# Optimization experiments

Hardware: AMD Instinct MI355X
Metric: run time of the kernel (lower is better)

## Reference

```python
import jax, jax.numpy as jnp
import numpy as np

B, M, H, E, N_ITEMS, N_USERS = 1024, 50, 128, 128, 100000, 1000


def setup_inputs() -> dict:
    key = jax.random.key(0)
    ks = jax.random.split(key, 16)
    s = 0.05
    return {
        "input_embedding": jax.random.normal(ks[0], (B, 1, E), jnp.float32),
        "hidden": jax.random.normal(ks[1], (1, B, H), jnp.float32),
        "inter_output": jax.random.normal(ks[2], (B, M, H), jnp.float32),
        "delta_t_h": jax.random.uniform(ks[3], (B,), jnp.float32),
        "user_list": jax.random.randint(ks[4], (B,), 0, N_USERS),
        # GRU params (input size 2*E since use_attn, single layer)
        "gru_w_ih": jax.random.normal(ks[5], (3 * H, 2 * E), jnp.float32) * s,
        "gru_w_hh": jax.random.normal(ks[6], (3 * H, H), jnp.float32) * s,
        "gru_b_ih": jax.random.normal(ks[7], (3 * H,), jnp.float32) * s,
        "gru_b_hh": jax.random.normal(ks[8], (3 * H,), jnp.float32) * s,
        # output projection
        "lin_W": jax.random.normal(ks[9], (N_ITEMS, H), jnp.float32) * s,
        "lin_b": jax.random.normal(ks[10], (N_ITEMS,), jnp.float32) * s,
        # per-user expert params ('cat' attention path)
        "cat_W": jax.random.normal(ks[11], (N_USERS, H, 2 * H), jnp.float32) * s,
        "cat_b": jax.random.normal(ks[12], (N_USERS, H), jnp.float32) * s,
        "scale_W": jax.random.normal(ks[13], (N_USERS, 1, H), jnp.float32) * s,
        "scale_b": jax.random.normal(ks[14], (N_USERS, 1), jnp.float32) * s,
    }


def reference(input_embedding, hidden, inter_output, delta_t_h, user_list,
              gru_w_ih, gru_w_hh, gru_b_ih, gru_b_hh,
              lin_W, lin_b, cat_W, cat_b, scale_W, scale_b):
    b, m, h = inter_output.shape
    # dropout in eval mode (p effectively 0) -> identity
    embedded_input = input_embedding
    hidden_t = jnp.transpose(hidden, (1, 0, 2))            # [B,1,H]
    # per-user 'cat' attention: gather each example's expert weights
    cat_in = jnp.concatenate(
        [jnp.broadcast_to(hidden_t, (b, m, h)), inter_output], axis=2)  # [B,M,2H]
    Wc = cat_W[user_list]                                   # [B,H,2H]
    bc = cat_b[user_list]                                   # [B,H]
    result = jnp.tanh(jnp.einsum('bmi,bhi->bmh', cat_in, Wc) + bc[:, None, :])
    Ws = scale_W[user_list]                                 # [B,1,H]
    bs = scale_b[user_list]                                 # [B,1]
    energies = jnp.einsum('bmh,boh->bmo', result, Ws) + bs[:, None, :]  # [B,M,1]
    attn_weights = jax.nn.softmax(energies[..., 0], axis=1)             # [B,M]
    context = jnp.einsum('bm,bmh->bh', attn_weights, inter_output)[:, None, :]  # [B,1,H]
    gru_in = jnp.concatenate([embedded_input, context], axis=2)         # [B,1,2E]
    # single-step GRU (PyTorch gate layout: r, z, n)
    x = gru_in[:, 0, :]
    h0 = hidden[0]                                          # [B,H]
    gi = x @ gru_w_ih.T + gru_b_ih                          # [B,3H]
    gh = h0 @ gru_w_hh.T + gru_b_hh
    i_r, i_z, i_n = jnp.split(gi, 3, axis=1)
    h_r, h_z, h_n = jnp.split(gh, 3, axis=1)
    r = jax.nn.sigmoid(i_r + h_r)
    z = jax.nn.sigmoid(i_z + h_z)
    n = jnp.tanh(i_n + r * h_n)
    h_new = (1.0 - z) * n + z * h0                          # [B,H]
    gru_output = h_new[:, None, :]                          # [B,1,H]
    output = gru_output @ lin_W.T + lin_b                   # [B,1,N_ITEMS]
    return (output, h_new[None], embedded_input, gru_output, attn_weights)
```

## Files before the change

kernel.cpp:

```cpp
#include <hip/hip_runtime.h>
#include <math.h>

#define NB 1024
#define NM 50
#define NH 128
#define NI 100000

constexpr size_t OFF_H   = (size_t)NB * NI;
constexpr size_t OFF_EMB = OFF_H   + (size_t)NB * NH;
constexpr size_t OFF_GRU = OFF_EMB + (size_t)NB * NH;
constexpr size_t OFF_ATT = OFF_GRU + (size_t)NB * NH;

#define CONV_BLOCKS 512

typedef __attribute__((ext_vector_type(8))) short bf16x8;
typedef __attribute__((ext_vector_type(4))) float f32x4;

static __device__ __forceinline__ unsigned short f2bf(float x) {
    unsigned int u = __float_as_uint(x);
    return (unsigned short)((u + 0x7FFFu + ((u >> 16) & 1u)) >> 16);
}
static __device__ __forceinline__ float bf2f(unsigned short v) {
    return __uint_as_float((unsigned int)v << 16);
}
static __device__ __forceinline__ float fast_tanh(float x) {
    float cx = fminf(fmaxf(x, -15.0f), 15.0f);
    float e = __expf(2.0f * cx);
    return (e - 1.0f) / (e + 1.0f);
}
static __device__ __forceinline__ float fast_sigmoid(float x) {
    float cx = fminf(fmaxf(x, -30.0f), 30.0f);
    return 1.0f / (1.0f + __expf(-cx));
}
static __device__ __forceinline__ bf16x8 pack8(float4 f0, float4 f1) {
    bf16x8 p;
    p[0] = (short)f2bf(f0.x); p[1] = (short)f2bf(f0.y);
    p[2] = (short)f2bf(f0.z); p[3] = (short)f2bf(f0.w);
    p[4] = (short)f2bf(f1.x); p[5] = (short)f2bf(f1.y);
    p[6] = (short)f2bf(f1.z); p[7] = (short)f2bf(f1.w);
    return p;
}

template<bool PRE>
__global__ __launch_bounds__(256) void attn_conv_split(
    const float* __restrict__ hidden,
    const float* __restrict__ inter,
    const int*   __restrict__ user_list,
    const float* __restrict__ cat_W,
    const float* __restrict__ cat_b,
    const float* __restrict__ scale_W,
    const float* __restrict__ lin_W,
    unsigned short* __restrict__ Wbf,
    float* __restrict__ attn_out,
    float* __restrict__ context)
{
    const int tid = threadIdx.x;

    if (blockIdx.x < CONV_BLOCKS) {
        if (PRE) {
            const int n8 = NI * NH / 8;
            for (int i = blockIdx.x * 256 + tid; i < n8; i += CONV_BLOCKS * 256) {
                const float* s = lin_W + (size_t)i * 8;
                bf16x8 p = pack8(*(const float4*)s, *(const float4*)(s + 4));
                __builtin_nontemporal_store(p, reinterpret_cast<bf16x8*>(Wbf + (size_t)i * 8));
            }
        }
        return;
    }

    const int b    = blockIdx.x - CONV_BLOCKS;
    const int lane = tid & 63;
    const int wave = tid >> 6;

    __shared__ __align__(16) unsigned short A[64 * 256];
    __shared__ float e_sm[64];
    __shared__ float attn_sm[64];

    const int u = user_list[b];

    for (int c = tid; c < 2048; c += 256) {
        int r = c >> 5, s = c & 31;
        float4 f0, f1;
        if (s < 16) {
            const float* src = hidden + (size_t)b * NH + s * 8;
            f0 = *(const float4*)src; f1 = *(const float4*)(src + 4);
        } else if (r < NM) {
            const float* src = inter + ((size_t)b * NM + r) * NH + (s - 16) * 8;
            f0 = *(const float4*)src; f1 = *(const float4*)(src + 4);
        } else {
            f0 = (float4){0,0,0,0}; f1 = f0;
        }
        int byte = (r * 512 + s * 16) ^ ((r & 7) << 4);
        *reinterpret_cast<bf16x8*>((char*)A + byte) = pack8(f0, f1);
    }
    if (tid < 64) e_sm[tid] = 0.0f;
    __syncthreads();

    const int lrow = lane & 15;
    const int lk8  = (lane >> 4) * 8;

    float bc[2], ws[2];
    #pragma unroll
    for (int nf = 0; nf < 2; ++nf) {
        int h = wave * 32 + nf * 16 + lrow;
        bc[nf] = cat_b[(size_t)u * NH + h];
        ws[nf] = scale_W[(size_t)u * NH + h];
    }

    f32x4 acc[4][2];
    #pragma unroll
    for (int mf = 0; mf < 4; ++mf)
        #pragma unroll
        for (int nf = 0; nf < 2; ++nf)
            acc[mf][nf] = (f32x4){0,0,0,0};

    #pragma unroll
    for (int ks = 0; ks < 8; ++ks) {
        bf16x8 bfr[2];
        #pragma unroll
        for (int nf = 0; nf < 2; ++nf) {
            int h = wave * 32 + nf * 16 + lrow;
            const float* wp = cat_W + ((size_t)u * NH + h) * 256 + ks * 32 + lk8;
            bfr[nf] = pack8(*(const float4*)wp, *(const float4*)(wp + 4));
        }
        #pragma unroll
        for (int mf = 0; mf < 4; ++mf) {
            int row  = mf * 16 + lrow;
            int byte = (row * 512 + ks * 64 + lk8 * 2) ^ ((row & 7) << 4);
            bf16x8 a = *reinterpret_cast<const bf16x8*>((char*)A + byte);
            acc[mf][0] = __builtin_amdgcn_mfma_f32_16x16x32_bf16(a, bfr[0], acc[mf][0], 0, 0, 0);
            acc[mf][1] = __builtin_amdgcn_mfma_f32_16x16x32_bf16(a, bfr[1], acc[mf][1], 0, 0, 0);
        }
    }

    #pragma unroll
    for (int mf = 0; mf < 4; ++mf) {
        #pragma unroll
        for (int j = 0; j < 4; ++j) {
            float s = fast_tanh(acc[mf][0][j] + bc[0]) * ws[0]
                    + fast_tanh(acc[mf][1][j] + bc[1]) * ws[1];
            s += __shfl_xor(s, 1); s += __shfl_xor(s, 2);
            s += __shfl_xor(s, 4); s += __shfl_xor(s, 8);
            if (lrow == 0) atomicAdd(&e_sm[mf * 16 + (lane >> 4) * 4 + j], s);
        }
    }
    __syncthreads();

    if (tid < 64) {
        float x = (tid < NM) ? e_sm[tid] : -INFINITY;
        float mx = x;
        #pragma unroll
        for (int s = 1; s < 64; s <<= 1) mx = fmaxf(mx, __shfl_xor(mx, s));
        float ex = (tid < NM) ? __expf(x - mx) : 0.0f;
        float sum = ex;
        #pragma unroll
        for (int s = 1; s < 64; s <<= 1) sum += __shfl_xor(sum, s);
        float aw = ex / sum;
        attn_sm[tid] = aw;
        if (tid < NM) attn_out[(size_t)b * NM + tid] = aw;
    }
    __syncthreads();

    if (tid < NH) {
        float c = 0.0f;
        #pragma unroll
        for (int m = 0; m < NM; ++m) {
            int byte = (m * 512 + (NH + tid) * 2) ^ ((m & 7) << 4);
            c = fmaf(attn_sm[m], bf2f(*reinterpret_cast<const unsigned short*>((char*)A + byte)), c);
        }
        context[(size_t)b * NH + tid] = c;
    }
}

__global__ __launch_bounds__(128) void gru_mfma(
    const float* __restrict__ emb,
    const float* __restrict__ hidden,
    const float* __restrict__ context,
    const float* __restrict__ w_ih,
    const float* __restrict__ w_hh,
    const float* __restrict__ b_ih,
    const float* __restrict__ b_hh,
    float* __restrict__ out_h,
    float* __restrict__ out_emb,
    float* __restrict__ out_gru)
{
    const int bg   = blockIdx.x >> 2;
    const int hc   = blockIdx.x & 3;
    const int b0   = bg * 16;
    const int h0   = hc * 32;
    const int tid  = threadIdx.x;
    const int lane = tid & 63;
    const int wave = tid >> 6;

    __shared__ __align__(16) unsigned short Xs[16 * 256];
    __shared__ __align__(16) unsigned short Hs[16 * 128];
    __shared__ float Gi[96][17];
    __shared__ float Gh[96][17];

    for (int c = tid; c < 768; c += 128) {
        if (c < 512) {
            int r = c >> 5, s = c & 31;
            const float* src = (s < 16)
                ? emb     + (size_t)(b0 + r) * NH + s * 8
                : context + (size_t)(b0 + r) * NH + (s - 16) * 8;
            int byte = (r * 512 + s * 16) ^ ((r & 7) << 4);
            *reinterpret_cast<bf16x8*>((char*)Xs + byte) =
                pack8(*(const float4*)src, *(const float4*)(src + 4));
        } else {
            int cc = c - 512;
            int r = cc >> 4, s = cc & 15;
            const float* src = hidden + (size_t)(b0 + r) * NH + s * 8;
            int byte = (r * 256 + s * 16) ^ ((r & 7) << 4);
            *reinterpret_cast<bf16x8*>((char*)Hs + byte) =
                pack8(*(const float4*)src, *(const float4*)(src + 4));
        }
    }
    __syncthreads();

    const int lrow = lane & 15;
    const int g16  = lane >> 4;
    const int lk8  = g16 * 8;

    bf16x8 xa[8], ha[4];
    #pragma unroll
    for (int ks = 0; ks < 8; ++ks) {
        int byte = (lrow * 512 + ks * 64 + lk8 * 2) ^ ((lrow & 7) << 4);
        xa[ks] = *reinterpret_cast<const bf16x8*>((char*)Xs + byte);
    }
    #pragma unroll
    for (int ks = 0; ks < 4; ++ks) {
        int byte = (lrow * 256 + ks * 64 + lk8 * 2) ^ ((lrow & 7) << 4);
        ha[ks] = *reinterpret_cast<const bf16x8*>((char*)Hs + byte);
    }

    #pragma unroll
    for (int f = 0; f < 3; ++f) {
        const int lb = (wave * 3 + f) * 16;
        const int l  = lb + lrow;
        const int gt = l >> 5;
        const int n  = gt * NH + h0 + (l & 31);
        f32x4 ai = (f32x4){0,0,0,0};
        f32x4 ah = (f32x4){0,0,0,0};
        const float* wi = w_ih + (size_t)n * 256;
        #pragma unroll
        for (int ks = 0; ks < 8; ++ks) {
            const float* wp = wi + ks * 32 + lk8;
            bf16x8 bv = pack8(*(const float4*)wp, *(const float4*)(wp + 4));
            ai = __builtin_amdgcn_mfma_f32_16x16x32_bf16(bv, xa[ks], ai, 0, 0, 0);
        }
        const float* wh = w_hh + (size_t)n * NH;
        #pragma unroll
        for (int ks = 0; ks < 4; ++ks) {
            const float* wp = wh + ks * 32 + lk8;
            bf16x8 bv = pack8(*(const float4*)wp, *(const float4*)(wp + 4));
            ah = __builtin_amdgcn_mfma_f32_16x16x32_bf16(bv, ha[ks], ah, 0, 0, 0);
        }
        #pragma unroll
        for (int j = 0; j < 4; ++j) {
            int lr = lb + g16 * 4 + j;
            Gi[lr][lrow] = ai[j];
            Gh[lr][lrow] = ah[j];
        }
    }
    __syncthreads();

    #pragma unroll
    for (int k = 0; k < 4; ++k) {
        int idx = k * 128 + tid;
        int bb  = idx >> 5;
        int hh  = idx & 31;
        int h   = h0 + hh;
        float gr = Gi[hh][bb]      + b_ih[h];
        float gz = Gi[32 + hh][bb] + b_ih[NH + h];
        float gn = Gi[64 + hh][bb] + b_ih[2 * NH + h];
        float hr = Gh[hh][bb]      + b_hh[h];
        float hz = Gh[32 + hh][bb] + b_hh[NH + h];
        float hn = Gh[64 + hh][bb] + b_hh[2 * NH + h];
        float r = fast_sigmoid(gr + hr);
        float z = fast_sigmoid(gz + hz);
        float n = fast_tanh(gn + r * hn);
        size_t o = (size_t)(b0 + bb) * NH + h;
        float h0v = hidden[o];
        float hnew = (1.0f - z) * n + z * h0v;
        out_h[o]   = hnew;
        out_gru[o] = hnew;
        out_emb[o] = emb[o];
    }
}

template<bool PRE>
__global__ __launch_bounds__(256, 4) void out_mfma(
    const float* __restrict__ hnew,
    const float* __restrict__ lin_W,
    const unsigned short* __restrict__ Wbf,
    const float* __restrict__ lin_b,
    float* __restrict__ out)
{
    const int L  = blockIdx.x;
    const int wg = (L & 7) * 782 + (L >> 3);
    const int mb = wg & 15;
    const int nb = wg >> 4;

    const int tid  = threadIdx.x;
    const int lane = tid & 63;
    const int wave = tid >> 6;

    const int b0 = mb * 64;
    const int n0 = nb * 256 + wave * 64;

    __shared__ __align__(16) unsigned char smem[32 * 260 * 4];
    unsigned short* As = (unsigned short*)smem;
    float (*Cs)[260]   = (float(*)[260])smem;

    for (int c = tid; c < 1024; c += 256) {
        int r = c >> 4;
        int s = c & 15;
        const float* src = hnew + (size_t)(b0 + r) * NH + s * 8;
        bf16x8 p = pack8(*(const float4*)src, *(const float4*)(src + 4));
        int byte = (r * 256 + s * 16) ^ ((r & 7) << 4);
        *reinterpret_cast<bf16x8*>((char*)As + byte) = p;
    }
    __syncthreads();

    const int lrow = lane & 15;
    const int g    = lane >> 4;
    const int lk8  = g * 8;

    f32x4 acc[4][4];
    #pragma unroll
    for (int mf = 0; mf < 4; ++mf)
        #pragma unroll
        for (int nf = 0; nf < 4; ++nf)
            acc[mf][nf] = (f32x4){0,0,0,0};

    #pragma unroll
    for (int ks = 0; ks < 4; ++ks) {
        bf16x8 av[4];
        #pragma unroll
        for (int mf = 0; mf < 4; ++mf) {
            int row  = mf * 16 + lrow;
            int byte = (row * 256 + ks * 64 + lk8 * 2) ^ ((row & 7) << 4);
            av[mf] = *reinterpret_cast<const bf16x8*>((char*)As + byte);
        }
        bf16x8 bv[4];
        #pragma unroll
        for (int nf = 0; nf < 4; ++nf) {
            int n = n0 + nf * 16 + lrow;
            const size_t nrow = (size_t)(n < NI ? n : 0) * NH;
            if (PRE) {
                bv[nf] = *reinterpret_cast<const bf16x8*>(Wbf + nrow + ks * 32 + lk8);
            } else {
                const float* wr = lin_W + nrow + ks * 32 + lk8;
                bv[nf] = pack8(*(const float4*)wr, *(const float4*)(wr + 4));
            }
        }
        #pragma unroll
        for (int nf = 0; nf < 4; ++nf)
            #pragma unroll
            for (int mf = 0; mf < 4; ++mf)
                acc[mf][nf] = __builtin_amdgcn_mfma_f32_16x16x32_bf16(
                    bv[nf], av[mf], acc[mf][nf], 0, 0, 0);
    }

    f32x4 bias4[4];
    #pragma unroll
    for (int nf = 0; nf < 4; ++nf) {
        int nq = n0 + nf * 16 + g * 4;
        if (nq > NI - 4) nq = NI - 4;
        const float4 bv = *(const float4*)(&lin_b[nq]);
        bias4[nf] = (f32x4){bv.x, bv.y, bv.z, bv.w};
    }

    #pragma unroll
    for (int half = 0; half < 2; ++half) {
        __syncthreads();
        #pragma unroll
        for (int mf2 = 0; mf2 < 2; ++mf2) {
            int mf = half * 2 + mf2;
            int rloc = mf2 * 16 + lrow;
            #pragma unroll
            for (int nf = 0; nf < 4; ++nf) {
                int colq = wave * 64 + nf * 16 + g * 4;
                *(f32x4*)(&Cs[rloc][colq]) = acc[mf][nf] + bias4[nf];
            }
        }
        __syncthreads();
        #pragma unroll
        for (int p = 0; p < 8; ++p) {
            int rloc = p * 4 + wave;
            int col4 = lane * 4;
            int n    = nb * 256 + col4;
            if (n < NI) {
                f32x4 v = *(const f32x4*)(&Cs[rloc][col4]);
                __builtin_nontemporal_store(v,
                    (f32x4*)(&out[(size_t)(b0 + half * 32 + rloc) * NI + n]));
            }
        }
    }
}

extern "C" void kernel_launch(void* const* d_in, const int* in_sizes, int n_in,
                              void* d_out, int out_size, void* d_ws, size_t ws_size,
                              hipStream_t stream) {
    const float* emb      = (const float*)d_in[0];
    const float* hidden   = (const float*)d_in[1];
    const float* inter    = (const float*)d_in[2];
    const int*   user     = (const int*)  d_in[4];
    const float* w_ih     = (const float*)d_in[5];
    const float* w_hh     = (const float*)d_in[6];
    const float* b_ih     = (const float*)d_in[7];
    const float* b_hh     = (const float*)d_in[8];
    const float* lin_W    = (const float*)d_in[9];
    const float* lin_b    = (const float*)d_in[10];
    const float* cat_W    = (const float*)d_in[11];
    const float* cat_b    = (const float*)d_in[12];
    const float* scale_W  = (const float*)d_in[13];

    float* out = (float*)d_out;
    const size_t wbf_bytes = (size_t)NI * NH * 2;
    const size_t need = wbf_bytes + 512 * 1024;
    const bool pre = (ws_size >= need);

    unsigned short* Wbf = (unsigned short*)d_ws;
    float* ctx = pre ? (float*)((char*)d_ws + wbf_bytes) : (float*)d_ws;

    if (pre) {
        attn_conv_split<true><<<CONV_BLOCKS + NB, 256, 0, stream>>>(
            hidden, inter, user, cat_W, cat_b, scale_W, lin_W, Wbf,
            out + OFF_ATT, ctx);
        gru_mfma<<<256, 128, 0, stream>>>(emb, hidden, ctx, w_ih, w_hh, b_ih, b_hh,
                                          out + OFF_H, out + OFF_EMB, out + OFF_GRU);
        out_mfma<true><<<6256, 256, 0, stream>>>(out + OFF_H, lin_W, Wbf, lin_b, out);
    } else {
        attn_conv_split<false><<<CONV_BLOCKS + NB, 256, 0, stream>>>(
            hidden, inter, user, cat_W, cat_b, scale_W, lin_W, nullptr,
            out + OFF_ATT, ctx);
        gru_mfma<<<256, 128, 0, stream>>>(emb, hidden, ctx, w_ih, w_hh, b_ih, b_hh,
                                          out + OFF_H, out + OFF_EMB, out + OFF_GRU);
        out_mfma<false><<<6256, 256, 0, stream>>>(out + OFF_H, lin_W, nullptr, lin_b, out);
    }
}
```

Measured before the change: 192.6 us.

## Retile output projection GEMM to 16 rows by 1024 item columns per block

The output projection kernel switches from 64x256 tiles to 16x1024 tiles. Each wave now computes a 16x256 strip with one A fragment and 16 B fragments, so each block writes 16 full 4 KB-wide row segments instead of 64 rows of 1 KB. The intent is longer contiguous output stores and fewer bias and A loads, in a kernel dominated by writing the 400 MB output. The cost is that each lin_W tile is reused across only 16 batch rows, so the weights are re-read from L2 four times as often. Every wave also holds all 16 accumulators live.

Result: slower. 304.8 us (+58.3%).

```diff
diff --git a/kernel.cpp b/kernel.cpp
--- a/kernel.cpp
+++ b/kernel.cpp
@@ -297,24 +297,22 @@
     float* __restrict__ out)
 {
     const int L  = blockIdx.x;
-    const int wg = (L & 7) * 782 + (L >> 3);
-    const int mb = wg & 15;
-    const int nb = wg >> 4;
+    const int wg = (L & 7) * 784 + (L >> 3);
+    const int mb = wg & 63;
+    const int nb = wg >> 6;
 
     const int tid  = threadIdx.x;
     const int lane = tid & 63;
     const int wave = tid >> 6;
 
-    const int b0 = mb * 64;
-    const int n0 = nb * 256 + wave * 64;
-
-    __shared__ __align__(16) unsigned char smem[32 * 260 * 4];
-    unsigned short* As = (unsigned short*)smem;
-    float (*Cs)[260]   = (float(*)[260])smem;
-
-    for (int c = tid; c < 1024; c += 256) {
-        int r = c >> 4;
-        int s = c & 15;
+    const int b0  = mb * 16;
+    const int n0w = nb * 1024 + wave * 256;
+
+    __shared__ __align__(16) unsigned short As[16 * 128];
+    __shared__ __align__(16) float Cs[8][1028];
+
+    {
+        int r = tid >> 4, s = tid & 15;
         const float* src = hnew + (size_t)(b0 + r) * NH + s * 8;
         bf16x8 p = pack8(*(const float4*)src, *(const float4*)(src + 4));
         int byte = (r * 256 + s * 16) ^ ((r & 7) << 4);
@@ -326,74 +324,52 @@
     const int g    = lane >> 4;
     const int lk8  = g * 8;
 
-    f32x4 acc[4][4];
-    #pragma unroll
-    for (int mf = 0; mf < 4; ++mf)
-        #pragma unroll
-        for (int nf = 0; nf < 4; ++nf)
-            acc[mf][nf] = (f32x4){0,0,0,0};
+    f32x4 acc[16];
+    #pragma unroll
+    for (int nf = 0; nf < 16; ++nf) acc[nf] = (f32x4){0,0,0,0};
 
     #pragma unroll
     for (int ks = 0; ks < 4; ++ks) {
-        bf16x8 av[4];
-        #pragma unroll
-        for (int mf = 0; mf < 4; ++mf) {
-            int row  = mf * 16 + lrow;
-            int byte = (row * 256 + ks * 64 + lk8 * 2) ^ ((row & 7) << 4);
-            av[mf] = *reinterpret_cast<const bf16x8*>((char*)As + byte);
-        }
-        bf16x8 bv[4];
-        #pragma unroll
-        for (int nf = 0; nf < 4; ++nf) {
-            int n = n0 + nf * 16 + lrow;
+        int abyte = (lrow * 256 + ks * 64 + lk8 * 2) ^ ((lrow & 7) << 4);
+        bf16x8 af = *reinterpret_cast<const bf16x8*>((char*)As + abyte);
+        #pragma unroll
+        for (int nf = 0; nf < 16; ++nf) {
+            int n = n0w + nf * 16 + lrow;
             const size_t nrow = (size_t)(n < NI ? n : 0) * NH;
+            bf16x8 bv;
             if (PRE) {
-                bv[nf] = *reinterpret_cast<const bf16x8*>(Wbf + nrow + ks * 32 + lk8);
+                bv = *reinterpret_cast<const bf16x8*>(Wbf + nrow + ks * 32 + lk8);
             } else {
                 const float* wr = lin_W + nrow + ks * 32 + lk8;
-                bv[nf] = pack8(*(const float4*)wr, *(const float4*)(wr + 4));
+                bv = pack8(*(const float4*)wr, *(const float4*)(wr + 4));
             }
-        }
-        #pragma unroll
-        for (int nf = 0; nf < 4; ++nf)
-            #pragma unroll
-            for (int mf = 0; mf < 4; ++mf)
-                acc[mf][nf] = __builtin_amdgcn_mfma_f32_16x16x32_bf16(
-                    bv[nf], av[mf], acc[mf][nf], 0, 0, 0);
-    }
-
-    f32x4 bias4[4];
-    #pragma unroll
-    for (int nf = 0; nf < 4; ++nf) {
-        int nq = n0 + nf * 16 + g * 4;
-        if (nq > NI - 4) nq = NI - 4;
-        const float4 bv = *(const float4*)(&lin_b[nq]);
-        bias4[nf] = (f32x4){bv.x, bv.y, bv.z, bv.w};
+            acc[nf] = __builtin_amdgcn_mfma_f32_16x16x32_bf16(bv, af, acc[nf], 0, 0, 0);
+        }
     }
 
     #pragma unroll
     for (int half = 0; half < 2; ++half) {
         __syncthreads();
-        #pragma unroll
-        for (int mf2 = 0; mf2 < 2; ++mf2) {
-            int mf = half * 2 + mf2;
-            int rloc = mf2 * 16 + lrow;
+        if ((lrow >> 3) == half) {
             #pragma unroll
-            for (int nf = 0; nf < 4; ++nf) {
-                int colq = wave * 64 + nf * 16 + g * 4;
-                *(f32x4*)(&Cs[rloc][colq]) = acc[mf][nf] + bias4[nf];
+            for (int nf = 0; nf < 16; ++nf) {
+                int nq  = n0w + nf * 16 + g * 4;
+                int nqc = (nq > NI - 4) ? (NI - 4) : nq;
+                const float4 bl = *(const float4*)(&lin_b[nqc]);
+                f32x4 v = acc[nf];
+                v[0] += bl.x; v[1] += bl.y; v[2] += bl.z; v[3] += bl.w;
+                *(f32x4*)(&Cs[lrow & 7][wave * 256 + nf * 16 + g * 4]) = v;
             }
         }
         __syncthreads();
         #pragma unroll
         for (int p = 0; p < 8; ++p) {
-            int rloc = p * 4 + wave;
-            int col4 = lane * 4;
-            int n    = nb * 256 + col4;
+            int col4 = tid * 4;
+            int n    = nb * 1024 + col4;
             if (n < NI) {
-                f32x4 v = *(const f32x4*)(&Cs[rloc][col4]);
+                f32x4 v = *(const f32x4*)(&Cs[p][col4]);
                 __builtin_nontemporal_store(v,
-                    (f32x4*)(&out[(size_t)(b0 + half * 32 + rloc) * NI + n]));
+                    (f32x4*)(&out[(size_t)(b0 + half * 8 + p) * NI + n]));
             }
         }
     }
@@ -430,13 +406,13 @@
             out + OFF_ATT, ctx);
         gru_mfma<<<256, 128, 0, stream>>>(emb, hidden, ctx, w_ih, w_hh, b_ih, b_hh,
                                           out + OFF_H, out + OFF_EMB, out + OFF_GRU);
-        out_mfma<true><<<6256, 256, 0, stream>>>(out + OFF_H, lin_W, Wbf, lin_b, out);
+        out_mfma<true><<<6272, 256, 0, stream>>>(out + OFF_H, lin_W, Wbf, lin_b, out);
     } else {
         attn_conv_split<false><<<CONV_BLOCKS + NB, 256, 0, stream>>>(
             hidden, inter, user, cat_W, cat_b, scale_W, lin_W, nullptr,
             out + OFF_ATT, ctx);
         gru_mfma<<<256, 128, 0, stream>>>(emb, hidden, ctx, w_ih, w_hh, b_ih, b_hh,
                                           out + OFF_H, out + OFF_EMB, out + OFF_GRU);
-        out_mfma<false><<<6256, 256, 0, stream>>>(out + OFF_H, lin_W, nullptr, lin_b, out);
-    }
-}
+        out_mfma<false><<<6272, 256, 0, stream>>>(out + OFF_H, lin_W, nullptr, lin_b, out);
+    }
+}
```
